# Optimization experiments

Hardware: AMD Instinct MI355X
Metric: run time of the kernel (lower is better)

## Reference

```python
import jax, jax.numpy as jnp
import numpy as np

N, E = 50000, 800000
NF, EF, HID, HEADS = 16, 8, 32, 4

def setup_inputs() -> dict:
    key = jax.random.key(0)
    ks = jax.random.split(key, 24)
    p = lambda k, shape: (jax.random.normal(k, shape, dtype=jnp.float32) * 0.1)
    HC = HID * HEADS  # 128
    return {
        "x": jax.random.normal(ks[0], (N, NF), dtype=jnp.float32),
        "edge_index": jax.random.randint(ks[1], (2, E), 0, N, dtype=jnp.int32),
        "edge_attr": jax.random.normal(ks[2], (E, EF), dtype=jnp.float32),
        # GAT layer 1: in NF -> heads=4, out=HID, concat
        "W1": p(ks[3], (NF, HC)), "aS1": p(ks[4], (HEADS, HID)), "aD1": p(ks[5], (HEADS, HID)), "b1": p(ks[6], (HC,)),
        # GAT layer 2: in HC -> heads=4, out=HID, concat
        "W2": p(ks[7], (HC, HC)), "aS2": p(ks[8], (HEADS, HID)), "aD2": p(ks[9], (HEADS, HID)), "b2": p(ks[10], (HC,)),
        # GAT layer 3: in HC -> heads=1, out=HID, mean (concat=False)
        "W3": p(ks[11], (HC, HID)), "aS3": p(ks[12], (1, HID)), "aD3": p(ks[13], (1, HID)), "b3": p(ks[14], (HID,)),
        # Edge MLP: Linear(2*HID+EF, HID) -> ReLU -> Linear(HID, 32) -> ReLU -> Linear(32, 1) -> Softplus
        "Wm1": p(ks[15], (2 * HID + EF, HID)), "bm1": p(ks[16], (HID,)),
        "Wm2": p(ks[17], (HID, 32)), "bm2": p(ks[18], (32,)),
        "Wm3": p(ks[19], (32, 1)), "bm3": p(ks[20], (1,)),
    }

def _gat_layer(x, src, dst, n, W, aS, aD, b, concat):
    # x:[N,Fin], W:[Fin,H*C], aS/aD:[H,C]
    H, C = aS.shape
    h = (x @ W).reshape(n, H, C)                       # [N,H,C]
    alpha_src = jnp.einsum('nhc,hc->nh', h, aS)        # [N,H]
    alpha_dst = jnp.einsum('nhc,hc->nh', h, aD)
    e = jax.nn.leaky_relu(alpha_src[src] + alpha_dst[dst], 0.2)  # [Et,H]
    # segment softmax over destination neighborhoods (self-loops guarantee coverage)
    m = jax.ops.segment_max(e, dst, num_segments=n)
    ex = jnp.exp(e - m[dst])
    s = jax.ops.segment_sum(ex, dst, num_segments=n)
    alpha = ex / (s[dst] + 1e-16)                      # [Et,H]
    msg = h[src] * alpha[:, :, None]                   # [Et,H,C]
    out = jax.ops.segment_sum(msg, dst, num_segments=n)  # [N,H,C]
    out = out.reshape(n, H * C) if concat else out.mean(axis=1)
    return out + b

def reference(x, edge_index, edge_attr, W1, aS1, aD1, b1, W2, aS2, aD2, b2, W3, aS3, aD3, b3, Wm1, bm1, Wm2, bm2, Wm3, bm3):
    n = x.shape[0]
    loop = jnp.arange(n, dtype=edge_index.dtype)
    src = jnp.concatenate([edge_index[0], loop])  # PyG GATConv adds self-loops by default
    dst = jnp.concatenate([edge_index[1], loop])
    h = jax.nn.elu(_gat_layer(x, src, dst, n, W1, aS1, aD1, b1, True))
    h = jax.nn.elu(_gat_layer(h, src, dst, n, W2, aS2, aD2, b2, True))
    h = _gat_layer(h, src, dst, n, W3, aS3, aD3, b3, False)   # [N,HID]
    ei = jnp.concatenate([h[edge_index[0]], h[edge_index[1]], edge_attr], axis=1)  # [E,2*HID+EF]
    z = jax.nn.relu(ei @ Wm1 + bm1)
    z = jax.nn.relu(z @ Wm2 + bm2)
    return jax.nn.softplus(z @ Wm3 + bm3)  # [E,1]
```

## Files before the change

kernel.cpp:

```cpp
#include <hip/hip_runtime.h>
#include <hip/hip_bf16.h>
#include <math.h>

#define N_NODES 50000
#define E_EDGES 800000
#define NFEAT 16
#define EFEAT 8
#define HID 32
#define HEADS 4
#define HC 128
#define SCAN_NB ((N_NODES + 255) / 256)

typedef float f4v __attribute__((ext_vector_type(4)));

__device__ __forceinline__ float lrelu(float v) { return v > 0.f ? v : 0.2f * v; }
__device__ __forceinline__ float bflo(unsigned u) { return __uint_as_float(u << 16); }
__device__ __forceinline__ float bfhi(unsigned u) { return __uint_as_float(u & 0xffff0000u); }
__device__ __forceinline__ f4v relu4(f4v v) {
    f4v r;
    r.x = v.x > 0.f ? v.x : 0.f;
    r.y = v.y > 0.f ? v.y : 0.f;
    r.z = v.z > 0.f ? v.z : 0.f;
    r.w = v.w > 0.f ? v.w : 0.f;
    return r;
}

template<int FIN, int HOUT, int H, bool BF16OUT, int NPT>
__global__ void k1_gemm_alpha(const float* __restrict__ x, const float* __restrict__ W,
                              const float* __restrict__ aS, const float* __restrict__ aD,
                              void* __restrict__ hout, float* __restrict__ asrc,
                              float* __restrict__ adst, int n_nodes)
{
    constexpr int GROUPS = 256 / HOUT;
    constexpr int NPB = GROUPS * NPT;
    constexpr bool SCALARX = (HOUT >= 64);
    __shared__ float xs[SCALARX ? 1 : NPB * (FIN + 1)];
    const int tid = threadIdx.x;
    const int nb0 = blockIdx.x * NPB;
    const int c = tid % HOUT;
    const int g = tid / HOUT;

    if constexpr (!SCALARX) {
        for (int idx = tid; idx < NPB * FIN; idx += 256) {
            int node = idx / FIN, k = idx % FIN;
            int gn = nb0 + node;
            xs[node * (FIN + 1) + k] = (gn < n_nodes) ? x[(size_t)gn * FIN + k] : 0.f;
        }
        __syncthreads();
    }

    const int head = c / HID;
    const int cc = c % HID;
    const float aSv = aS[head * HID + cc];
    const float aDv = aD[head * HID + cc];
    float acc[NPT];
#pragma unroll
    for (int i = 0; i < NPT; i++) acc[i] = 0.f;

    if constexpr (SCALARX) {
        const float* xr[NPT];
#pragma unroll
        for (int i = 0; i < NPT; i++) {
            int n = nb0 + g * NPT + i;
            unsigned nu = (unsigned)__builtin_amdgcn_readfirstlane(n < n_nodes ? n : 0);
            xr[i] = x + (size_t)nu * FIN;
        }
#pragma unroll 8
        for (int k = 0; k < FIN; k++) {
            float w = W[k * HOUT + c];
#pragma unroll
            for (int i = 0; i < NPT; i++) acc[i] += w * xr[i][k];
        }
    } else {
        for (int k = 0; k < FIN; k++) {
            float w = W[k * HOUT + c];
#pragma unroll
            for (int i = 0; i < NPT; i++)
                acc[i] += w * xs[(g * NPT + i) * (FIN + 1) + k];
        }
    }

#pragma unroll
    for (int i = 0; i < NPT; i++) {
        int n = nb0 + g * NPT + i;
        bool ok = (n < n_nodes);
        float h = acc[i];
        if (ok) {
            if (BF16OUT)
                ((__hip_bfloat16*)hout)[(size_t)n * HOUT + c] = __float2bfloat16(h);
            else
                ((float*)hout)[(size_t)n * HOUT + c] = h;
        }
        float pa = h * aSv, pb = h * aDv;
#pragma unroll
        for (int off = 16; off >= 1; off >>= 1) {
            pa += __shfl_xor(pa, off, 32);
            pb += __shfl_xor(pb, off, 32);
        }
        if (ok && cc == 0) { asrc[n * H + head] = pa; adst[n * H + head] = pb; }
    }
}

__global__ void kc_count(const int* __restrict__ ei1, int* __restrict__ cnt,
                         int* __restrict__ rank)
{
    int e = blockIdx.x * 256 + threadIdx.x;
    if (e >= E_EDGES) return;
    rank[e] = atomicAdd(&cnt[ei1[e]], 1);
}

__global__ __launch_bounds__(256) void kc_blocksum(const int* __restrict__ cnt,
                                                   int* __restrict__ bsum)
{
    __shared__ int sd[256];
    const int tid = threadIdx.x;
    int i = blockIdx.x * 256 + tid;
    int v = (i < N_NODES) ? cnt[i] : 0;
    sd[tid] = v;
    __syncthreads();
    for (int off = 128; off >= 1; off >>= 1) {
        if (tid < off) sd[tid] += sd[tid + off];
        __syncthreads();
    }
    if (tid == 0) bsum[blockIdx.x] = sd[0];
}

__global__ __launch_bounds__(256) void kc_scanbsum(const int* __restrict__ bsum,
                                                   int* __restrict__ bofs)
{
    __shared__ int sd[256];
    const int tid = threadIdx.x;
    int v = (tid < SCAN_NB) ? bsum[tid] : 0;
    sd[tid] = v;
    __syncthreads();
    for (int off = 1; off < 256; off <<= 1) {
        int u = (tid >= off) ? sd[tid - off] : 0;
        __syncthreads();
        sd[tid] += u;
        __syncthreads();
    }
    if (tid < SCAN_NB) bofs[tid] = sd[tid] - v;
}

__global__ __launch_bounds__(256) void kc_apply(const int* __restrict__ cnt,
                                                const int* __restrict__ bofs,
                                                int* __restrict__ rowptr)
{
    __shared__ int sd[256];
    const int tid = threadIdx.x;
    int i = blockIdx.x * 256 + tid;
    int v = (i < N_NODES) ? cnt[i] : 0;
    sd[tid] = v;
    __syncthreads();
    for (int off = 1; off < 256; off <<= 1) {
        int u = (tid >= off) ? sd[tid - off] : 0;
        __syncthreads();
        sd[tid] += u;
        __syncthreads();
    }
    int excl = sd[tid] - v + bofs[blockIdx.x];
    if (i < N_NODES) rowptr[i] = excl;
}

__global__ void kc_scatter(const int* __restrict__ ei0, const int* __restrict__ ei1,
                           const int* __restrict__ rowptr, const int* __restrict__ rank,
                           int* __restrict__ srcs)
{
    int e = blockIdx.x * 256 + threadIdx.x;
    if (e >= E_EDGES) return;
    srcs[rowptr[ei1[e]] + rank[e]] = ei0[e];
}

template<int H, int C, bool DO_ELU, bool BF16H>
__global__ __launch_bounds__(256) void k_aggr(
    const float* __restrict__ asrc, const float* __restrict__ adst,
    const void* __restrict__ hbuf, const int* __restrict__ rowptr,
    const int* __restrict__ deg, const int* __restrict__ srcs,
    const float* __restrict__ b, float* __restrict__ outp)
{
    constexpr int HCL = H * C;
    constexpr int TPE = HCL / 2;
    constexpr int NPB = 256 / TPE;
    constexpr bool UNI = (TPE == 64);
    const int t = threadIdx.x % TPE;
    const int n = blockIdx.x * NPB + threadIdx.x / TPE;
    if (n >= N_NODES) return;
    const int c0 = 2 * t;
    const int head = c0 / C;
    const float adstv = adst[n * H + head];
    const unsigned* hbu = (const unsigned*)hbuf;
    const float* hbf = (const float*)hbuf;
    const float m0 = lrelu(asrc[n * H + head] + adstv);
    float ssum = 1.f;
    float a0, a1;
    if (BF16H) {
        unsigned u = hbu[(size_t)n * TPE + t];
        a0 = bflo(u); a1 = bfhi(u);
    } else {
        float2 hv = *(const float2*)(hbf + (size_t)n * HCL + c0);
        a0 = hv.x; a1 = hv.y;
    }
    const int base = rowptr[n];
    const int dg = deg[n];
    int i = 0;

    if constexpr (UNI && BF16H) {
        for (; i + 8 <= dg; i += 8) {
            int s[8];
#pragma unroll
            for (int u = 0; u < 8; u++)
                s[u] = __builtin_amdgcn_readfirstlane(srcs[base + i + u]);
            float ex[8];
#pragma unroll
            for (int u = 0; u < 8; u++)
                ex[u] = __expf(lrelu(asrc[s[u] * H + head] + adstv) - m0);
            unsigned hu[8];
#pragma unroll
            for (int u = 0; u < 8; u++)
                hu[u] = hbu[(size_t)s[u] * TPE + t];
#pragma unroll
            for (int u = 0; u < 8; u++) {
                ssum += ex[u];
                a0 += ex[u] * bflo(hu[u]);
                a1 += ex[u] * bfhi(hu[u]);
            }
        }
    }

    for (; i + 4 <= dg; i += 4) {
        int s0 = srcs[base + i + 0];
        int s1 = srcs[base + i + 1];
        int s2 = srcs[base + i + 2];
        int s3 = srcs[base + i + 3];
        if (UNI) {
            s0 = __builtin_amdgcn_readfirstlane(s0);
            s1 = __builtin_amdgcn_readfirstlane(s1);
            s2 = __builtin_amdgcn_readfirstlane(s2);
            s3 = __builtin_amdgcn_readfirstlane(s3);
        }
        float ex[4];
        ex[0] = __expf(lrelu(asrc[s0 * H + head] + adstv) - m0);
        ex[1] = __expf(lrelu(asrc[s1 * H + head] + adstv) - m0);
        ex[2] = __expf(lrelu(asrc[s2 * H + head] + adstv) - m0);
        ex[3] = __expf(lrelu(asrc[s3 * H + head] + adstv) - m0);
        float hx[4], hy[4];
        if (BF16H) {
            unsigned u0 = hbu[(size_t)s0 * TPE + t];
            unsigned u1 = hbu[(size_t)s1 * TPE + t];
            unsigned u2 = hbu[(size_t)s2 * TPE + t];
            unsigned u3 = hbu[(size_t)s3 * TPE + t];
            hx[0] = bflo(u0); hy[0] = bfhi(u0);
            hx[1] = bflo(u1); hy[1] = bfhi(u1);
            hx[2] = bflo(u2); hy[2] = bfhi(u2);
            hx[3] = bflo(u3); hy[3] = bfhi(u3);
        } else {
            float2 h0 = *(const float2*)(hbf + (size_t)s0 * HCL + c0);
            float2 h1 = *(const float2*)(hbf + (size_t)s1 * HCL + c0);
            float2 h2 = *(const float2*)(hbf + (size_t)s2 * HCL + c0);
            float2 h3 = *(const float2*)(hbf + (size_t)s3 * HCL + c0);
            hx[0] = h0.x; hy[0] = h0.y;
            hx[1] = h1.x; hy[1] = h1.y;
            hx[2] = h2.x; hy[2] = h2.y;
            hx[3] = h3.x; hy[3] = h3.y;
        }
#pragma unroll
        for (int u = 0; u < 4; u++) {
            ssum += ex[u];
            a0 += ex[u] * hx[u];
            a1 += ex[u] * hy[u];
        }
    }
    for (; i < dg; i++) {
        int s = srcs[base + i];
        if (UNI) s = __builtin_amdgcn_readfirstlane(s);
        float ex = __expf(lrelu(asrc[s * H + head] + adstv) - m0);
        float hxv, hyv;
        if (BF16H) {
            unsigned u = hbu[(size_t)s * TPE + t];
            hxv = bflo(u); hyv = bfhi(u);
        } else {
            float2 hs = *(const float2*)(hbf + (size_t)s * HCL + c0);
            hxv = hs.x; hyv = hs.y;
        }
        ssum += ex;
        a0 += ex * hxv;
        a1 += ex * hyv;
    }
    float inv = 1.f / (ssum + 1e-16f);
    float v0 = a0 * inv + b[c0];
    float v1 = a1 * inv + b[c0 + 1];
    if (DO_ELU) {
        v0 = v0 > 0.f ? v0 : __expf(v0) - 1.f;
        v1 = v1 > 0.f ? v1 : __expf(v1) - 1.f;
    }
    *(float2*)(outp + (size_t)n * HCL + c0) = make_float2(v0, v1);
}

__global__ __launch_bounds__(256) void k5a_precomp(
    const float* __restrict__ h3, const float* __restrict__ Wm1,
    __hip_bfloat16* __restrict__ Pb)
{
    __shared__ __align__(16) float w[64 * 32];
    __shared__ __align__(16) float hsh[16][33];
    const int tid = threadIdx.x;
    for (int i = tid; i < 64 * 32; i += 256) w[i] = Wm1[i];
    const int nb0 = blockIdx.x * 16;
    for (int idx = tid; idx < 16 * 32; idx += 256) {
        int node = idx / 32, k = idx % 32;
        int gn = nb0 + node;
        hsh[node][k] = (gn < N_NODES) ? h3[gn * 32 + k] : 0.f;
    }
    __syncthreads();
    const int c = tid % 64;
    const int part = c / 32;
    const int j = c % 32;
    for (int ln = tid / 64; ln < 16; ln += 4) {
        int gn = nb0 + ln;
        if (gn >= N_NODES) break;
        float sum = 0.f;
#pragma unroll
        for (int k = 0; k < 32; k++)
            sum += hsh[ln][k] * w[(part * 32 + k) * 32 + j];
        Pb[(size_t)gn * 64 + c] = __float2bfloat16(sum);
    }
}

__global__ __launch_bounds__(256, 4) void k5b_mlp(
                       const int* __restrict__ ei0, const int* __restrict__ ei1,
                       const __hip_bfloat16* __restrict__ Pb, const float* __restrict__ ea,
                       const float* __restrict__ Wm1, const float* __restrict__ bm1,
                       const float* __restrict__ Wm2, const float* __restrict__ bm2,
                       const float* __restrict__ Wm3, const float* __restrict__ bm3,
                       float* __restrict__ out)
{
    const int e = blockIdx.x * 256 + threadIdx.x;
    if (e >= E_EDGES) return;
    const int s = ei0[e], d = ei1[e];

    const f4v* bm1v = (const f4v*)bm1;
    f4v z1v[8];
#pragma unroll
    for (int q = 0; q < 8; q++) z1v[q] = bm1v[q];

    const f4v* eav = (const f4v*)(ea + (size_t)e * 8);
#pragma unroll
    for (int kq = 0; kq < 2; kq++) {
        f4v v = eav[kq];
#pragma unroll
        for (int r = 0; r < 4; r++) {
            float vr = (r == 0) ? v.x : (r == 1) ? v.y : (r == 2) ? v.z : v.w;
            const f4v* w4 = (const f4v*)(Wm1 + (64 + kq * 4 + r) * 32);
#pragma unroll
            for (int q = 0; q < 8; q++) z1v[q] += w4[q] * vr;
        }
    }
    const uint4* ps4 = (const uint4*)(Pb + (size_t)s * 64);
    const uint4* pd4 = (const uint4*)(Pb + (size_t)d * 64 + 32);
#pragma unroll
    for (int q = 0; q < 4; q++) {
        uint4 a = ps4[q];
        uint4 b = pd4[q];
        f4v pa0 = {bflo(a.x), bfhi(a.x), bflo(a.y), bfhi(a.y)};
        f4v pa1 = {bflo(a.z), bfhi(a.z), bflo(a.w), bfhi(a.w)};
        f4v pb0 = {bflo(b.x), bfhi(b.x), bflo(b.y), bfhi(b.y)};
        f4v pb1 = {bflo(b.z), bfhi(b.z), bflo(b.w), bfhi(b.w)};
        z1v[2 * q + 0] += pa0 + pb0;
        z1v[2 * q + 1] += pa1 + pb1;
    }
#pragma unroll
    for (int q = 0; q < 8; q++) z1v[q] = relu4(z1v[q]);

    const f4v* bm2v = (const f4v*)bm2;
    f4v acc2v[8];
#pragma unroll
    for (int q = 0; q < 8; q++) acc2v[q] = bm2v[q];
#pragma unroll
    for (int k = 0; k < 32; k++) {
        float zk = z1v[k >> 2][k & 3];
        const f4v* w4 = (const f4v*)(Wm2 + k * 32);
#pragma unroll
        for (int q = 0; q < 8; q++) acc2v[q] += w4[q] * zk;
    }
    float z3 = bm3[0];
#pragma unroll
    for (int q = 0; q < 8; q++) {
        const float* w3q = Wm3 + 4 * q;
        float c0 = acc2v[q].x, c1 = acc2v[q].y, c2 = acc2v[q].z, c3 = acc2v[q].w;
        z3 += (c0 > 0.f ? c0 : 0.f) * w3q[0];
        z3 += (c1 > 0.f ? c1 : 0.f) * w3q[1];
        z3 += (c2 > 0.f ? c2 : 0.f) * w3q[2];
        z3 += (c3 > 0.f ? c3 : 0.f) * w3q[3];
    }

    float r = (z3 > 20.f) ? z3 : log1pf(__expf(z3));
    __builtin_nontemporal_store(r, &out[e]);
}

extern "C" void kernel_launch(void* const* d_in, const int* in_sizes, int n_in,
                              void* d_out, int out_size, void* d_ws, size_t ws_size,
                              hipStream_t stream)
{
    const float* x   = (const float*)d_in[0];
    const int*   ei  = (const int*)d_in[1];
    const int*   ei0 = ei;
    const int*   ei1 = ei + E_EDGES;
    const float* ea  = (const float*)d_in[2];
    const float* W1  = (const float*)d_in[3];
    const float* aS1 = (const float*)d_in[4];
    const float* aD1 = (const float*)d_in[5];
    const float* b1  = (const float*)d_in[6];
    const float* W2  = (const float*)d_in[7];
    const float* aS2 = (const float*)d_in[8];
    const float* aD2 = (const float*)d_in[9];
    const float* b2  = (const float*)d_in[10];
    const float* W3  = (const float*)d_in[11];
    const float* aS3 = (const float*)d_in[12];
    const float* aD3 = (const float*)d_in[13];
    const float* b3  = (const float*)d_in[14];
    const float* Wm1 = (const float*)d_in[15];
    const float* bm1 = (const float*)d_in[16];
    const float* Wm2 = (const float*)d_in[17];
    const float* bm2 = (const float*)d_in[18];
    const float* Wm3 = (const float*)d_in[19];
    const float* bm3 = (const float*)d_in[20];

    float* ws = (float*)d_ws;
    float* bufA = ws;
    float* bufB = bufA + (size_t)N_NODES * HC;
    float* asrc = bufB + (size_t)N_NODES * HC;
    float* adst = asrc + (size_t)N_NODES * HEADS;
    int* cnt    = (int*)(adst + (size_t)N_NODES * HEADS);
    int* rowptr = cnt + N_NODES;
    int* rank   = rowptr + N_NODES;
    int* srcs   = rank + E_EDGES;
    int* bsum   = srcs + E_EDGES;
    int* bofs   = bsum + 256;

    float* out = (float*)d_out;

    hipMemsetAsync(cnt, 0, (size_t)N_NODES * sizeof(int), stream);
    kc_count<<<(E_EDGES + 255) / 256, 256, 0, stream>>>(ei1, cnt, rank);
    kc_blocksum<<<SCAN_NB, 256, 0, stream>>>(cnt, bsum);
    kc_scanbsum<<<1, 256, 0, stream>>>(bsum, bofs);
    kc_apply<<<SCAN_NB, 256, 0, stream>>>(cnt, bofs, rowptr);
    kc_scatter<<<(E_EDGES + 255) / 256, 256, 0, stream>>>(ei0, ei1, rowptr, rank, srcs);

    k1_gemm_alpha<NFEAT, HC, HEADS, true, 4><<<(N_NODES + 7) / 8, 256, 0, stream>>>(
        x, W1, aS1, aD1, bufA, asrc, adst, N_NODES);
    k_aggr<HEADS, HID, true, true><<<(N_NODES + 3) / 4, 256, 0, stream>>>(
        asrc, adst, bufA, rowptr, cnt, srcs, b1, bufB);

    k1_gemm_alpha<HC, HC, HEADS, true, 8><<<(N_NODES + 15) / 16, 256, 0, stream>>>(
        bufB, W2, aS2, aD2, bufA, asrc, adst, N_NODES);
    k_aggr<HEADS, HID, true, true><<<(N_NODES + 3) / 4, 256, 0, stream>>>(
        asrc, adst, bufA, rowptr, cnt, srcs, b2, bufB);

    k1_gemm_alpha<HC, HID, 1, false, 4><<<(N_NODES + 31) / 32, 256, 0, stream>>>(
        bufB, W3, aS3, aD3, bufA, asrc, adst, N_NODES);
    k_aggr<1, HID, false, false><<<(N_NODES + 15) / 16, 256, 0, stream>>>(
        asrc, adst, bufA, rowptr, cnt, srcs, b3, bufB);

    __hip_bfloat16* Pb = (__hip_bfloat16*)bufA;
    k5a_precomp<<<(N_NODES + 15) / 16, 256, 0, stream>>>(bufB, Wm1, Pb);
    k5b_mlp<<<(E_EDGES + 255) / 256, 256, 0, stream>>>(
        ei0, ei1, Pb, ea, Wm1, bm1, Wm2, bm2, Wm3, bm3, out);
}
```

Before: 312.4 us.

## Compute layer-2 GEMM with bf16 MFMA and separate alpha kernel

Layer-1 aggregation now writes its output in bf16, and the layer-2 128x128 projection runs on MFMA 16x16x32 bf16 instructions using a pre-transposed bf16 copy of W2. The attention logits are then computed by a separate small kernel that reads the bf16 projection. The goal is to cut the FP32 scalar GEMM cost and halve the intermediate activation traffic. In exchange it adds two launches, an extra pass over the bf16 hidden features, and bf16 rounding of layer-2 inputs. The MFMA kernel also writes scattered single-bf16 stores.

```diff
diff --git a/kernel.cpp b/kernel.cpp
--- a/kernel.cpp
+++ b/kernel.cpp
@@ -12,6 +12,7 @@
 #define SCAN_NB ((N_NODES + 255) / 256)
 
 typedef float f4v __attribute__((ext_vector_type(4)));
+typedef short short8 __attribute__((ext_vector_type(8)));
 
 __device__ __forceinline__ float lrelu(float v) { return v > 0.f ? v : 0.2f * v; }
 __device__ __forceinline__ float bflo(unsigned u) { return __uint_as_float(u << 16); }
@@ -98,6 +99,75 @@
             pb += __shfl_xor(pb, off, 32);
         }
         if (ok && cc == 0) { asrc[n * H + head] = pa; adst[n * H + head] = pb; }
+    }
+}
+
+__global__ __launch_bounds__(256) void kw_conv(const float* __restrict__ W2,
+                                               short* __restrict__ W2T)
+{
+    int idx = blockIdx.x * 256 + threadIdx.x;
+    if (idx >= HC * HC) return;
+    int c = idx >> 7, k = idx & 127;
+    __hip_bfloat16 v = __float2bfloat16(W2[k * HC + c]);
+    W2T[idx] = (short)__hip_bfloat16_raw(v).x;
+}
+
+__global__ __launch_bounds__(256) void k1_mfma(
+    const __hip_bfloat16* __restrict__ xb,
+    const short* __restrict__ W2T,
+    __hip_bfloat16* __restrict__ hout)
+{
+    const int wave = threadIdx.x >> 6;
+    const int lane = threadIdx.x & 63;
+    const int tile = blockIdx.x * 4 + wave;
+    if (tile >= N_NODES / 16) return;
+    const int m0 = tile * 16;
+    const int l15 = lane & 15;
+    const int kb = lane >> 4;
+    short8 a[4];
+    const short* xrow = (const short*)(xb + (size_t)(m0 + l15) * HC);
+#pragma unroll
+    for (int kt = 0; kt < 4; kt++)
+        a[kt] = *(const short8*)(xrow + kt * 32 + kb * 8);
+#pragma unroll
+    for (int ct = 0; ct < 8; ct++) {
+        const short* wrow = W2T + (size_t)(ct * 16 + l15) * HC;
+        f4v acc = {0.f, 0.f, 0.f, 0.f};
+#pragma unroll
+        for (int kt = 0; kt < 4; kt++) {
+            short8 bfr = *(const short8*)(wrow + kt * 32 + kb * 8);
+            acc = __builtin_amdgcn_mfma_f32_16x16x32_bf16(a[kt], bfr, acc, 0, 0, 0);
+        }
+#pragma unroll
+        for (int r = 0; r < 4; r++) {
+            int node = m0 + kb * 4 + r;
+            int ch = ct * 16 + l15;
+            hout[(size_t)node * HC + ch] = __float2bfloat16(acc[r]);
+        }
+    }
+}
+
+__global__ __launch_bounds__(256) void k_alpha(
+    const unsigned* __restrict__ hb,
+    const float* __restrict__ aS, const float* __restrict__ aD,
+    float* __restrict__ asrc, float* __restrict__ adst)
+{
+    const int lane = threadIdx.x & 63;
+    const int n = blockIdx.x * 4 + (threadIdx.x >> 6);
+    if (n >= N_NODES) return;
+    unsigned u = hb[(size_t)n * 64 + lane];
+    float h0 = bflo(u), h1 = bfhi(u);
+    float pa = h0 * aS[2 * lane] + h1 * aS[2 * lane + 1];
+    float pb = h0 * aD[2 * lane] + h1 * aD[2 * lane + 1];
+#pragma unroll
+    for (int off = 8; off >= 1; off >>= 1) {
+        pa += __shfl_xor(pa, off, 64);
+        pb += __shfl_xor(pb, off, 64);
+    }
+    if ((lane & 15) == 0) {
+        int head = lane >> 4;
+        asrc[n * HEADS + head] = pa;
+        adst[n * HEADS + head] = pb;
     }
 }
 
@@ -171,12 +241,12 @@
     srcs[rowptr[ei1[e]] + rank[e]] = ei0[e];
 }
 
-template<int H, int C, bool DO_ELU, bool BF16H>
+template<int H, int C, bool DO_ELU, bool BF16H, bool OBF16>
 __global__ __launch_bounds__(256) void k_aggr(
     const float* __restrict__ asrc, const float* __restrict__ adst,
     const void* __restrict__ hbuf, const int* __restrict__ rowptr,
     const int* __restrict__ deg, const int* __restrict__ srcs,
-    const float* __restrict__ b, float* __restrict__ outp)
+    const float* __restrict__ b, void* __restrict__ outp)
 {
     constexpr int HCL = H * C;
     constexpr int TPE = HCL / 2;
@@ -293,7 +363,13 @@
         v0 = v0 > 0.f ? v0 : __expf(v0) - 1.f;
         v1 = v1 > 0.f ? v1 : __expf(v1) - 1.f;
     }
-    *(float2*)(outp + (size_t)n * HCL + c0) = make_float2(v0, v1);
+    if constexpr (OBF16) {
+        __hip_bfloat16* ob = (__hip_bfloat16*)outp;
+        ob[(size_t)n * HCL + c0]     = __float2bfloat16(v0);
+        ob[(size_t)n * HCL + c0 + 1] = __float2bfloat16(v1);
+    } else {
+        *(float2*)((float*)outp + (size_t)n * HCL + c0) = make_float2(v0, v1);
+    }
 }
 
 __global__ __launch_bounds__(256) void k5a_precomp(
@@ -435,11 +511,13 @@
     int* srcs   = rank + E_EDGES;
     int* bsum   = srcs + E_EDGES;
     int* bofs   = bsum + 256;
+    short* W2T  = (short*)(bofs + 256);
 
     float* out = (float*)d_out;
 
     hipMemsetAsync(cnt, 0, (size_t)N_NODES * sizeof(int), stream);
     kc_count<<<(E_EDGES + 255) / 256, 256, 0, stream>>>(ei1, cnt, rank);
+    kw_conv<<<(HC * HC + 255) / 256, 256, 0, stream>>>(W2, W2T);
     kc_blocksum<<<SCAN_NB, 256, 0, stream>>>(cnt, bsum);
     kc_scanbsum<<<1, 256, 0, stream>>>(bsum, bofs);
     kc_apply<<<SCAN_NB, 256, 0, stream>>>(cnt, bofs, rowptr);
@@ -447,17 +525,19 @@
 
     k1_gemm_alpha<NFEAT, HC, HEADS, true, 4><<<(N_NODES + 7) / 8, 256, 0, stream>>>(
         x, W1, aS1, aD1, bufA, asrc, adst, N_NODES);
-    k_aggr<HEADS, HID, true, true><<<(N_NODES + 3) / 4, 256, 0, stream>>>(
+    k_aggr<HEADS, HID, true, true, true><<<(N_NODES + 3) / 4, 256, 0, stream>>>(
         asrc, adst, bufA, rowptr, cnt, srcs, b1, bufB);
 
-    k1_gemm_alpha<HC, HC, HEADS, true, 8><<<(N_NODES + 15) / 16, 256, 0, stream>>>(
-        bufB, W2, aS2, aD2, bufA, asrc, adst, N_NODES);
-    k_aggr<HEADS, HID, true, true><<<(N_NODES + 3) / 4, 256, 0, stream>>>(
+    k1_mfma<<<(N_NODES / 16 + 3) / 4, 256, 0, stream>>>(
+        (const __hip_bfloat16*)bufB, W2T, (__hip_bfloat16*)bufA);
+    k_alpha<<<(N_NODES + 3) / 4, 256, 0, stream>>>(
+        (const unsigned*)bufA, aS2, aD2, asrc, adst);
+    k_aggr<HEADS, HID, true, true, false><<<(N_NODES + 3) / 4, 256, 0, stream>>>(
         asrc, adst, bufA, rowptr, cnt, srcs, b2, bufB);
 
     k1_gemm_alpha<HC, HID, 1, false, 4><<<(N_NODES + 31) / 32, 256, 0, stream>>>(
         bufB, W3, aS3, aD3, bufA, asrc, adst, N_NODES);
-    k_aggr<1, HID, false, false><<<(N_NODES + 15) / 16, 256, 0, stream>>>(
+    k_aggr<1, HID, false, false, false><<<(N_NODES + 15) / 16, 256, 0, stream>>>(
         asrc, adst, bufA, rowptr, cnt, srcs, b3, bufB);
 
     __hip_bfloat16* Pb = (__hip_bfloat16*)bufA;
```

Measured after the change: 291.3 us. 6.7% less time.
